# Optimization experiments

Hardware: AMD Instinct MI355X
Metric: run time of the kernel (lower is better)

Reference implementation:

```python
import jax, jax.numpy as jnp
import numpy as np

B, S, D = 2, 512, 64

def setup_inputs() -> dict:
    key = jax.random.key(0)
    k1, k2, k3, k4, k5 = jax.random.split(key, 5)
    x = jax.random.normal(k1, (B, S, D, D), dtype=jnp.float32)
    log_A = jax.random.normal(k2, (D,), dtype=jnp.float32) * 0.02
    # nn.Linear(dim, 1): weight (1, dim) -> store as (dim,), bias scalar
    dt_w = jax.random.normal(k3, (D,), dtype=jnp.float32) * (1.0 / np.sqrt(D))
    dt_b = jax.random.normal(k4, (), dtype=jnp.float32) * (1.0 / np.sqrt(D))
    # LayerNorm over normalized_shape=(dim, dim)
    ln_w = jnp.ones((D, D), dtype=jnp.float32)
    ln_b = jnp.zeros((D, D), dtype=jnp.float32)
    return {"x": x, "log_A": log_A, "dt_w": dt_w, "dt_b": dt_b, "ln_w": ln_w, "ln_b": ln_b}

def _layernorm_2d(x, w, b, eps=1e-5):
    # normalize over last two dims (d, d)
    mu = jnp.mean(x, axis=(-2, -1), keepdims=True)
    var = jnp.var(x, axis=(-2, -1), keepdims=True)
    return (x - mu) * jax.lax.rsqrt(var + eps) * w + b

def reference(x, log_A, dt_w, dt_b, ln_w, ln_b):
    b, seq, d, _ = x.shape
    x_in = x
    xn = _layernorm_2d(x, ln_w, ln_b)                      # (b, s, d, d)
    A_cont = -jnp.exp(log_A)                               # (d,)
    dt = jax.nn.softplus(jnp.einsum('bsdc,c->bsd', xn, dt_w) + dt_b)  # (b, s, d)
    log_A_dt = dt * A_cont                                 # (b, s, d)
    cs = jnp.cumsum(log_A_dt, axis=1)                      # (b, s, d)
    log_M = cs[:, :, None, :] - cs[:, None, :, :]          # (b, t, j, d)
    idx = jnp.arange(seq)
    mask = (idx[:, None] >= idx[None, :])[None, :, :, None]  # causal (1, t, j, 1)
    M = jnp.exp(jnp.where(mask, log_M, -jnp.inf))          # (b, t, j, d)
    out = jnp.einsum('btjr,bjrc->btrc', M, xn)             # (b, t, d, d)
    return out + x_in
```

## Files before the change

### kernel.cpp

```cpp
#include <hip/hip_runtime.h>
#include <math.h>

#define BB 2
#define SS 512
#define DD 64
#define DDDD 4096

__global__ __launch_bounds__(256) void k1_stats(
    const float* __restrict__ x, const float* __restrict__ log_A,
    const float* __restrict__ dt_w, const float* __restrict__ dt_b,
    const float* __restrict__ ln_w, const float* __restrict__ ln_b,
    float* __restrict__ a_out, float2* __restrict__ stats)
{
    const int bs  = blockIdx.x;
    const int tid = threadIdx.x;

    const float4* xp4 = (const float4*)(x + (size_t)bs * DDDD + tid * 16);
    float4 v0 = xp4[0], v1 = xp4[1], v2 = xp4[2], v3 = xp4[3];

    float sum = (v0.x+v0.y+v0.z+v0.w) + (v1.x+v1.y+v1.z+v1.w)
              + (v2.x+v2.y+v2.z+v2.w) + (v3.x+v3.y+v3.z+v3.w);
    float sq  = (v0.x*v0.x+v0.y*v0.y+v0.z*v0.z+v0.w*v0.w)
              + (v1.x*v1.x+v1.y*v1.y+v1.z*v1.z+v1.w*v1.w)
              + (v2.x*v2.x+v2.y*v2.y+v2.z*v2.z+v2.w*v2.w)
              + (v3.x*v3.x+v3.y*v3.y+v3.z*v3.z+v3.w*v3.w);

    #pragma unroll
    for (int off = 32; off > 0; off >>= 1) {
        sum += __shfl_down(sum, off);
        sq  += __shfl_down(sq,  off);
    }
    __shared__ float s_sum[4], s_sq[4];
    const int wv = tid >> 6, ln = tid & 63;
    if (ln == 0) { s_sum[wv] = sum; s_sq[wv] = sq; }
    __syncthreads();
    const float tsum = s_sum[0] + s_sum[1] + s_sum[2] + s_sum[3];
    const float tsq  = s_sq[0]  + s_sq[1]  + s_sq[2]  + s_sq[3];
    const float mu   = tsum * (1.0f / DDDD);
    const float var  = tsq  * (1.0f / DDDD) - mu * mu;
    const float rstd = rsqrtf(var + 1e-5f);

    const float4* lw4 = (const float4*)(ln_w + tid * 16);
    const float4* lb4 = (const float4*)(ln_b + tid * 16);
    const float4* dw4 = (const float4*)(dt_w + (tid & 3) * 16);
    float p = 0.f;
    #define ACC4(vv, ii) { \
        float4 lw = lw4[ii], lb = lb4[ii], dw = dw4[ii];            \
        p = fmaf(fmaf((vv.x - mu) * rstd, lw.x, lb.x), dw.x, p);    \
        p = fmaf(fmaf((vv.y - mu) * rstd, lw.y, lb.y), dw.y, p);    \
        p = fmaf(fmaf((vv.z - mu) * rstd, lw.z, lb.z), dw.z, p);    \
        p = fmaf(fmaf((vv.w - mu) * rstd, lw.w, lb.w), dw.w, p);    \
    }
    ACC4(v0, 0); ACC4(v1, 1); ACC4(v2, 2); ACC4(v3, 3);
    #undef ACC4

    p += __shfl_xor(p, 1);
    p += __shfl_xor(p, 2);

    if ((tid & 3) == 0) {
        const int d = tid >> 2;
        float z = p + dt_b[0];
        float dt = (z > 20.f) ? z : log1pf(expf(z));
        float la = dt * (-expf(log_A[d]));
        a_out[bs * DD + d] = expf(la);
    }
    if (tid == 0) stats[bs] = make_float2(mu, rstd);
}

#define NW 8
#define CH (SS / NW)

__global__ __launch_bounds__(512) void k2_scan(
    const float* __restrict__ x, const float* __restrict__ a_in,
    const float* __restrict__ ln_w, const float* __restrict__ ln_b,
    const float2* __restrict__ stats, float* __restrict__ out)
{
    const int br  = blockIdx.x;
    const int b   = br >> 6, r = br & 63;
    const int tid = threadIdx.x;
    const int w   = tid >> 6;
    const int c   = tid & 63;

    const float lnw = ln_w[r * DD + c];
    const float lnb = ln_b[r * DD + c];

    const int t0 = w * CH;
    const size_t xbase = ((size_t)(b * SS) * DD + r) * DD + c;
    const float*  xp = x   + xbase + (size_t)t0 * DDDD;
    const float*  ap = a_in + (b * SS + t0) * DD + r;
    const float2* sp = stats + b * SS + t0;

    float state = 0.f, P = 1.f;
    for (int t = 0; t < CH; t += 8) {
        float xv[8], av[8]; float2 st[8];
        #pragma unroll
        for (int i = 0; i < 8; ++i) {
            xv[i] = xp[(size_t)(t + i) * DDDD];
            av[i] = ap[(t + i) * DD];
            st[i] = sp[t + i];
        }
        #pragma unroll
        for (int i = 0; i < 8; ++i) {
            float xn = fmaf((xv[i] - st[i].x) * st[i].y, lnw, lnb);
            state = fmaf(av[i], state, xn);
            P *= av[i];
        }
    }

    __shared__ float sF[NW][DD];
    __shared__ float sP[NW];
    sF[w][c] = state;
    if (c == 0) sP[w] = P;
    __syncthreads();

    float carry = 0.f;
    for (int v = 0; v < w; ++v) carry = fmaf(sP[v], carry, sF[v][c]);

    state = carry;
    float* op = out + xbase + (size_t)t0 * DDDD;
    for (int t = 0; t < CH; t += 8) {
        float xv[8], av[8]; float2 st[8];
        #pragma unroll
        for (int i = 0; i < 8; ++i) {
            xv[i] = xp[(size_t)(t + i) * DDDD];
            av[i] = ap[(t + i) * DD];
            st[i] = sp[t + i];
        }
        #pragma unroll
        for (int i = 0; i < 8; ++i) {
            float xn = fmaf((xv[i] - st[i].x) * st[i].y, lnw, lnb);
            state = fmaf(av[i], state, xn);
            op[(size_t)(t + i) * DDDD] = state + xv[i];
        }
    }
}

extern "C" void kernel_launch(void* const* d_in, const int* in_sizes, int n_in,
                              void* d_out, int out_size, void* d_ws, size_t ws_size,
                              hipStream_t stream) {
    const float* x     = (const float*)d_in[0];
    const float* log_A = (const float*)d_in[1];
    const float* dt_w  = (const float*)d_in[2];
    const float* dt_b  = (const float*)d_in[3];
    const float* ln_w  = (const float*)d_in[4];
    const float* ln_b  = (const float*)d_in[5];
    float* out = (float*)d_out;

    float*  a_buf = (float*)d_ws;
    float2* stats = (float2*)((char*)d_ws + (size_t)BB * SS * DD * sizeof(float));

    k1_stats<<<BB * SS, 256, 0, stream>>>(x, log_A, dt_w, dt_b, ln_w, ln_b, a_buf, stats);
    k2_scan<<<BB * DD, 512, 0, stream>>>(x, a_buf, ln_w, ln_b, stats, out);
}
```

Baseline: 92.43 us.

## Split chunked scan into two kernels with 16 chunks per row

Replaces the single scan kernel, which ran 128 blocks of 8 chunk-waves, with a partial-sum kernel and a finalize kernel. Each uses 16 chunks per (batch,row), giving 512 blocks of 4 waves. The chunk carries now pass through a global workspace instead of shared memory. This raises parallelism to better fill the GPU's compute units, at the cost of an extra kernel launch and global round-trips for the carries.

```diff
diff --git a/kernel.cpp b/kernel.cpp
--- a/kernel.cpp
+++ b/kernel.cpp
@@ -5,6 +5,8 @@
 #define SS 512
 #define DD 64
 #define DDDD 4096
+#define NC 16
+#define CL (SS / NC)
 
 __global__ __launch_bounds__(256) void k1_stats(
     const float* __restrict__ x, const float* __restrict__ log_A,
@@ -67,31 +69,28 @@
     if (tid == 0) stats[bs] = make_float2(mu, rstd);
 }
 
-#define NW 8
-#define CH (SS / NW)
-
-__global__ __launch_bounds__(512) void k2_scan(
+__global__ __launch_bounds__(256) void k2a_partial(
     const float* __restrict__ x, const float* __restrict__ a_in,
     const float* __restrict__ ln_w, const float* __restrict__ ln_b,
-    const float2* __restrict__ stats, float* __restrict__ out)
+    const float2* __restrict__ stats,
+    float* __restrict__ Fbuf, float* __restrict__ Pbuf)
 {
-    const int br  = blockIdx.x;
-    const int b   = br >> 6, r = br & 63;
-    const int tid = threadIdx.x;
-    const int w   = tid >> 6;
-    const int c   = tid & 63;
+    const int gw = blockIdx.x * 4 + (threadIdx.x >> 6);
+    const int c  = threadIdx.x & 63;
+    const int ch = gw & (NC - 1);
+    const int br = gw >> 4;
+    const int b  = br >> 6, r = br & 63;
 
     const float lnw = ln_w[r * DD + c];
     const float lnb = ln_b[r * DD + c];
 
-    const int t0 = w * CH;
-    const size_t xbase = ((size_t)(b * SS) * DD + r) * DD + c;
-    const float*  xp = x   + xbase + (size_t)t0 * DDDD;
+    const int t0 = ch * CL;
+    const float*  xp = x + (((size_t)(b * SS + t0)) * DD + r) * DD + c;
     const float*  ap = a_in + (b * SS + t0) * DD + r;
     const float2* sp = stats + b * SS + t0;
 
     float state = 0.f, P = 1.f;
-    for (int t = 0; t < CH; t += 8) {
+    for (int t = 0; t < CL; t += 8) {
         float xv[8], av[8]; float2 st[8];
         #pragma unroll
         for (int i = 0; i < 8; ++i) {
@@ -106,19 +105,49 @@
             P *= av[i];
         }
     }
+    Fbuf[(size_t)gw * DD + c] = state;
+    if (c == 0) Pbuf[gw] = P;
+}
 
-    __shared__ float sF[NW][DD];
-    __shared__ float sP[NW];
-    sF[w][c] = state;
-    if (c == 0) sP[w] = P;
-    __syncthreads();
+__global__ __launch_bounds__(256) void k2b_final(
+    const float* __restrict__ x, const float* __restrict__ a_in,
+    const float* __restrict__ ln_w, const float* __restrict__ ln_b,
+    const float2* __restrict__ stats,
+    const float* __restrict__ Fbuf, const float* __restrict__ Pbuf,
+    float* __restrict__ out)
+{
+    const int gw = blockIdx.x * 4 + (threadIdx.x >> 6);
+    const int c  = threadIdx.x & 63;
+    const int ch = gw & (NC - 1);
+    const int br = gw >> 4;
+    const int b  = br >> 6, r = br & 63;
 
+    float f[NC], p[NC];
+    #pragma unroll
+    for (int v = 0; v < NC; ++v) {
+        f[v] = Fbuf[(size_t)(br * NC + v) * DD + c];
+        p[v] = Pbuf[br * NC + v];
+    }
     float carry = 0.f;
-    for (int v = 0; v < w; ++v) carry = fmaf(sP[v], carry, sF[v][c]);
+    #pragma unroll
+    for (int v = 0; v < NC; ++v) {
+        float pv = (v < ch) ? p[v] : 1.f;
+        float fv = (v < ch) ? f[v] : 0.f;
+        carry = fmaf(pv, carry, fv);
+    }
 
-    state = carry;
-    float* op = out + xbase + (size_t)t0 * DDDD;
-    for (int t = 0; t < CH; t += 8) {
+    const float lnw = ln_w[r * DD + c];
+    const float lnb = ln_b[r * DD + c];
+
+    const int t0 = ch * CL;
+    const size_t xoff = (((size_t)(b * SS + t0)) * DD + r) * DD + c;
+    const float*  xp = x + xoff;
+    const float*  ap = a_in + (b * SS + t0) * DD + r;
+    const float2* sp = stats + b * SS + t0;
+    float* op = out + xoff;
+
+    float state = carry;
+    for (int t = 0; t < CL; t += 8) {
         float xv[8], av[8]; float2 st[8];
         #pragma unroll
         for (int i = 0; i < 8; ++i) {
@@ -146,9 +175,13 @@
     const float* ln_b  = (const float*)d_in[5];
     float* out = (float*)d_out;
 
-    float*  a_buf = (float*)d_ws;
-    float2* stats = (float2*)((char*)d_ws + (size_t)BB * SS * DD * sizeof(float));
+    char* ws = (char*)d_ws;
+    float*  a_buf = (float*)ws;
+    float2* stats = (float2*)(ws + 262144);
+    float*  Fbuf  = (float*)(ws + 262144 + 8192);
+    float*  Pbuf  = (float*)(ws + 262144 + 8192 + 524288);
 
     k1_stats<<<BB * SS, 256, 0, stream>>>(x, log_A, dt_w, dt_b, ln_w, ln_b, a_buf, stats);
-    k2_scan<<<BB * DD, 512, 0, stream>>>(x, a_buf, ln_w, ln_b, stats, out);
+    k2a_partial<<<BB * DD * NC / 4, 256, 0, stream>>>(x, a_buf, ln_w, ln_b, stats, Fbuf, Pbuf);
+    k2b_final<<<BB * DD * NC / 4, 256, 0, stream>>>(x, a_buf, ln_w, ln_b, stats, Fbuf, Pbuf, out);
 }
```

New measurement: 89.88 us. -2.8%, faster.
